# Kernel tuning notes

Measured on AMD Instinct MI355X. Metric: run time of the kernel, lower is better.

The kernel has to match this reference:

```python
import jax, jax.numpy as jnp
import numpy as np

N_NODES = 100000
N_EDGES = 1600000
D_IN = 256
D_OUT = 64
AVG_DEG = N_EDGES // N_NODES  # 16


def setup_inputs() -> dict:
    key = jax.random.key(0)
    k1, k2, k3 = jax.random.split(key, 3)
    X = jax.random.normal(k1, (N_NODES, D_IN), dtype=jnp.float32)
    weights = jax.random.normal(k2, (D_IN, D_OUT), dtype=jnp.float32) * (1.0 / np.sqrt(D_IN))
    # CSR with uniform degree for a valid structure (load balance is a kernel concern, not math)
    row_pointers = jnp.arange(N_NODES + 1, dtype=jnp.int64) * AVG_DEG
    column_index = jax.random.randint(k3, (N_EDGES,), 0, N_NODES, dtype=jnp.int64)
    # GNNAdvisor precomputes degrees as d^{-1/2} for symmetric GCN normalization
    deg = (row_pointers[1:] - row_pointers[:-1]).astype(jnp.float32)
    degrees = 1.0 / jnp.sqrt(jnp.maximum(deg, 1.0))
    return {"X": X, "weights": weights, "row_pointers": row_pointers,
            "column_index": column_index, "degrees": degrees}


def reference(X, weights, row_pointers, column_index, degrees):
    # Dense transform: [N, D_in] @ [D_in, D_out] -> [N, D_out]
    X_prime = jnp.matmul(X, weights)
    E = column_index.shape[0]
    # CSR row ids for each edge (destination node of the aggregation)
    row_ids = jnp.searchsorted(row_pointers, jnp.arange(E, dtype=row_pointers.dtype), side='right') - 1
    # out[i] = d_i^{-1/2} * sum_{j in N(i)} d_j^{-1/2} * X'[j]
    gathered = X_prime[column_index] * degrees[column_index][:, None]  # [E, D_out]
    agg = jax.ops.segment_sum(gathered, row_ids, num_segments=row_pointers.shape[0] - 1)
    return agg * degrees[:, None]
```

## Files before the change

### kernel.cpp

```cpp
#include <hip/hip_runtime.h>
#include <hip/hip_bf16.h>


constexpr int D_IN  = 256;
constexpr int D_OUT = 64;
constexpr int WT_LD = D_IN + 8;

typedef short  s8v  __attribute__((ext_vector_type(8)));
typedef __bf16 bf8v __attribute__((ext_vector_type(8)));
typedef float  f32x4 __attribute__((ext_vector_type(4)));
typedef unsigned short us8v __attribute__((ext_vector_type(8)));

union BF8 { bf8v b; s8v s; };

__global__ void prep_w_kernel(const float* __restrict__ W,
                              unsigned short* __restrict__ Wt_g)
{
    const int c = blockIdx.x;
    const int k = threadIdx.x;
    __bf16 b = (__bf16)W[(size_t)k * D_OUT + c];
    Wt_g[(size_t)c * D_IN + k] = *reinterpret_cast<unsigned short*>(&b);
}

__global__ __launch_bounds__(256) void gemm_bf16_kernel(
    const float* __restrict__ X, const unsigned short* __restrict__ Wt_g,
    const float* __restrict__ deg, unsigned short* __restrict__ Xp,
    int n, int ntiles)
{
    __shared__ unsigned short Wt[D_OUT][WT_LD];

    const int tid = threadIdx.x;

    {
        const int c = tid >> 2, seg = tid & 3;
        const us8v* src = reinterpret_cast<const us8v*>(Wt_g + (size_t)c * D_IN + seg * 64);
        us8v* dst = reinterpret_cast<us8v*>(&Wt[c][seg * 64]);
        #pragma unroll
        for (int i = 0; i < 8; ++i) dst[i] = src[i];
    }
    __syncthreads();

    const int wid  = tid >> 6;
    const int lane = tid & 63;
    const int lrow = lane & 15;
    const int kgrp = lane >> 4;

    const unsigned short* wt0 = &Wt[lrow][kgrp * 8];
    const int wstride = gridDim.x << 2;

    for (int tile = blockIdx.x * 4 + wid; tile < ntiles; tile += wstride) {
        const int grow = tile * 16 + lrow;
        const int xr   = grow < n ? grow : n - 1;
        const float* xrow = X + (size_t)xr * D_IN + kgrp * 8;

        f32x4 acc[4] = {};

        #pragma unroll
        for (int ks = 0; ks < 8; ++ks) {
            const float4 x0 = *reinterpret_cast<const float4*>(xrow + ks * 32);
            const float4 x1 = *reinterpret_cast<const float4*>(xrow + ks * 32 + 4);
            BF8 xf;
            xf.b[0] = (__bf16)x0.x; xf.b[1] = (__bf16)x0.y;
            xf.b[2] = (__bf16)x0.z; xf.b[3] = (__bf16)x0.w;
            xf.b[4] = (__bf16)x1.x; xf.b[5] = (__bf16)x1.y;
            xf.b[6] = (__bf16)x1.z; xf.b[7] = (__bf16)x1.w;

            #pragma unroll
            for (int f = 0; f < 4; ++f) {
                const s8v wf = *reinterpret_cast<const s8v*>(
                    wt0 + (size_t)f * 16 * WT_LD + ks * 32);
                acc[f] = __builtin_amdgcn_mfma_f32_16x16x32_bf16(wf, xf.s, acc[f], 0, 0, 0);
            }
        }

        if (grow < n) {
            const float d = deg[grow];
            #pragma unroll
            for (int f = 0; f < 4; ++f) {
                ushort4 v;
                __bf16 b0 = (__bf16)(acc[f][0] * d);
                __bf16 b1 = (__bf16)(acc[f][1] * d);
                __bf16 b2 = (__bf16)(acc[f][2] * d);
                __bf16 b3 = (__bf16)(acc[f][3] * d);
                v.x = *reinterpret_cast<unsigned short*>(&b0);
                v.y = *reinterpret_cast<unsigned short*>(&b1);
                v.z = *reinterpret_cast<unsigned short*>(&b2);
                v.w = *reinterpret_cast<unsigned short*>(&b3);
                *reinterpret_cast<ushort4*>(
                    &Xp[(size_t)grow * D_OUT + f * 16 + kgrp * 4]) = v;
            }
        }
    }
}

__global__ __launch_bounds__(256) void agg_kernel(
    const unsigned short* __restrict__ Xp, const int* __restrict__ rp,
    const int* __restrict__ ci, const float* __restrict__ deg,
    float* __restrict__ out, int n)
{
    const int node = blockIdx.x * 32 + (threadIdx.x >> 3);
    if (node >= n) return;
    const int c8 = (threadIdx.x & 7) * 8;

    const int e0 = rp[node];
    const int e1 = rp[node + 1];
    const int m  = e1 - e0;

    float acc[8] = {};

    if (m == 16 && (e0 & 3) == 0) {
        int4 i4[4];
        #pragma unroll
        for (int b = 0; b < 4; ++b)
            i4[b] = *reinterpret_cast<const int4*>(&ci[e0 + b * 4]);
        const int idx[16] = { i4[0].x, i4[0].y, i4[0].z, i4[0].w,
                              i4[1].x, i4[1].y, i4[1].z, i4[1].w,
                              i4[2].x, i4[2].y, i4[2].z, i4[2].w,
                              i4[3].x, i4[3].y, i4[3].z, i4[3].w };
        us8v v[16];
        #pragma unroll
        for (int j = 0; j < 16; ++j)
            v[j] = *reinterpret_cast<const us8v*>(&Xp[(size_t)idx[j] * D_OUT + c8]);
        #pragma unroll
        for (int j = 0; j < 16; ++j) {
            #pragma unroll
            for (int k = 0; k < 8; ++k)
                acc[k] += __uint_as_float((unsigned)v[j][k] << 16);
        }
    } else {
        for (int e = e0; e < e1; ++e) {
            const us8v v = *reinterpret_cast<const us8v*>(&Xp[(size_t)ci[e] * D_OUT + c8]);
            #pragma unroll
            for (int k = 0; k < 8; ++k)
                acc[k] += __uint_as_float((unsigned)v[k] << 16);
        }
    }

    const float d = deg[node];
    float* op = out + (size_t)node * D_OUT + c8;
    *reinterpret_cast<float4*>(op)     = make_float4(acc[0]*d, acc[1]*d, acc[2]*d, acc[3]*d);
    *reinterpret_cast<float4*>(op + 4) = make_float4(acc[4]*d, acc[5]*d, acc[6]*d, acc[7]*d);
}

extern "C" void kernel_launch(void* const* d_in, const int* in_sizes, int n_in,
                              void* d_out, int out_size, void* d_ws, size_t ws_size,
                              hipStream_t stream)
{
    const float* X   = (const float*)d_in[0];
    const float* W   = (const float*)d_in[1];
    const int*   rp  = (const int*)d_in[2];
    const int*   ci  = (const int*)d_in[3];
    const float* deg = (const float*)d_in[4];
    float* out = (float*)d_out;

    const int n = in_sizes[4];

    unsigned short* Xp   = (unsigned short*)d_ws;
    unsigned short* Wt_g = (unsigned short*)((char*)d_ws + (16u << 20));

    prep_w_kernel<<<D_OUT, D_IN, 0, stream>>>(W, Wt_g);

    const int ntiles = (n + 15) / 16;
    gemm_bf16_kernel<<<391, 256, 0, stream>>>(X, Wt_g, deg, Xp, n, ntiles);

    const int agg_blocks = (n + 31) / 32;
    agg_kernel<<<agg_blocks, 256, 0, stream>>>(Xp, rp, ci, deg, out, n);
}
```

Before: 60.36 us.

## Pre-swizzle weights into MFMA fragment order and load via global_load_lds

The weight prep kernel now writes bf16 weights in the exact per-lane MFMA fragment layout, so the GEMM kernel can copy them straight into LDS with global_load_lds and read conflict-free contiguous 16-byte fragments. The GEMM switches from a persistent grid-stride loop to one tile per wave with a launch sized to the tile count, and issues all 16 X float4 loads up front before converting and multiplying. This aims to raise memory-level parallelism on the X stream and cut LDS staging overhead, in exchange for more blocks each reloading the 32KB weight tile into LDS. The agg kernel also hoists the degree load earlier.

After: 59.00 us. 1.02x faster.

```diff
diff --git a/kernel.cpp b/kernel.cpp
--- a/kernel.cpp
+++ b/kernel.cpp
@@ -4,7 +4,6 @@
 
 constexpr int D_IN  = 256;
 constexpr int D_OUT = 64;
-constexpr int WT_LD = D_IN + 8;
 
 typedef short  s8v  __attribute__((ext_vector_type(8)));
 typedef __bf16 bf8v __attribute__((ext_vector_type(8)));
@@ -16,10 +15,20 @@
 __global__ void prep_w_kernel(const float* __restrict__ W,
                               unsigned short* __restrict__ Wt_g)
 {
-    const int c = blockIdx.x;
-    const int k = threadIdx.x;
-    __bf16 b = (__bf16)W[(size_t)k * D_OUT + c];
-    Wt_g[(size_t)c * D_IN + k] = *reinterpret_cast<unsigned short*>(&b);
+    const int t     = blockIdx.x * 256 + threadIdx.x;
+    const int lane  = t & 63;
+    const int chunk = t >> 6;
+    const int ks    = chunk >> 2;
+    const int f     = chunk & 3;
+    const int col   = f * 16 + (lane & 15);
+    const int k0    = (lane >> 4) * 8 + ks * 32;
+    us8v v;
+    #pragma unroll
+    for (int i = 0; i < 8; ++i) {
+        __bf16 b = (__bf16)W[(size_t)(k0 + i) * D_OUT + col];
+        v[i] = *reinterpret_cast<unsigned short*>(&b);
+    }
+    *reinterpret_cast<us8v*>(Wt_g + (size_t)t * 8) = v;
 }
 
 __global__ __launch_bounds__(256) void gemm_bf16_kernel(
@@ -27,68 +36,73 @@
     const float* __restrict__ deg, unsigned short* __restrict__ Xp,
     int n, int ntiles)
 {
-    __shared__ unsigned short Wt[D_OUT][WT_LD];
+    __shared__ unsigned short Wt[32 * 512];
 
-    const int tid = threadIdx.x;
+    const int tid  = threadIdx.x;
+    const int wid  = tid >> 6;
+    const int lane = tid & 63;
 
-    {
-        const int c = tid >> 2, seg = tid & 3;
-        const us8v* src = reinterpret_cast<const us8v*>(Wt_g + (size_t)c * D_IN + seg * 64);
-        us8v* dst = reinterpret_cast<us8v*>(&Wt[c][seg * 64]);
-        #pragma unroll
-        for (int i = 0; i < 8; ++i) dst[i] = src[i];
+    #pragma unroll
+    for (int c = 0; c < 8; ++c) {
+        const int chunk = wid * 8 + c;
+        const unsigned short* src = Wt_g + (size_t)chunk * 512 + lane * 8;
+        __builtin_amdgcn_global_load_lds(
+            (const __attribute__((address_space(1))) void*)src,
+            (__attribute__((address_space(3))) void*)&Wt[chunk * 512],
+            16, 0, 0);
     }
     __syncthreads();
 
-    const int wid  = tid >> 6;
-    const int lane = tid & 63;
+    const int tile = blockIdx.x * 4 + wid;
+    if (tile >= ntiles) return;
+
     const int lrow = lane & 15;
     const int kgrp = lane >> 4;
+    const int grow = tile * 16 + lrow;
+    const int xr   = grow < n ? grow : n - 1;
+    const float* xrow = X + (size_t)xr * D_IN + kgrp * 8;
 
-    const unsigned short* wt0 = &Wt[lrow][kgrp * 8];
-    const int wstride = gridDim.x << 2;
+    float4 xv[16];
+    #pragma unroll
+    for (int ks = 0; ks < 8; ++ks) {
+        xv[2 * ks]     = *reinterpret_cast<const float4*>(xrow + ks * 32);
+        xv[2 * ks + 1] = *reinterpret_cast<const float4*>(xrow + ks * 32 + 4);
+    }
 
-    for (int tile = blockIdx.x * 4 + wid; tile < ntiles; tile += wstride) {
-        const int grow = tile * 16 + lrow;
-        const int xr   = grow < n ? grow : n - 1;
-        const float* xrow = X + (size_t)xr * D_IN + kgrp * 8;
-
-        f32x4 acc[4] = {};
+    f32x4 acc[4] = {};
+    #pragma unroll
+    for (int ks = 0; ks < 8; ++ks) {
+        BF8 xf;
+        const float4 x0 = xv[2 * ks];
+        const float4 x1 = xv[2 * ks + 1];
+        xf.b[0] = (__bf16)x0.x; xf.b[1] = (__bf16)x0.y;
+        xf.b[2] = (__bf16)x0.z; xf.b[3] = (__bf16)x0.w;
+        xf.b[4] = (__bf16)x1.x; xf.b[5] = (__bf16)x1.y;
+        xf.b[6] = (__bf16)x1.z; xf.b[7] = (__bf16)x1.w;
 
         #pragma unroll
-        for (int ks = 0; ks < 8; ++ks) {
-            const float4 x0 = *reinterpret_cast<const float4*>(xrow + ks * 32);
-            const float4 x1 = *reinterpret_cast<const float4*>(xrow + ks * 32 + 4);
-            BF8 xf;
-            xf.b[0] = (__bf16)x0.x; xf.b[1] = (__bf16)x0.y;
-            xf.b[2] = (__bf16)x0.z; xf.b[3] = (__bf16)x0.w;
-            xf.b[4] = (__bf16)x1.x; xf.b[5] = (__bf16)x1.y;
-            xf.b[6] = (__bf16)x1.z; xf.b[7] = (__bf16)x1.w;
+        for (int f = 0; f < 4; ++f) {
+            const s8v wf = *reinterpret_cast<const s8v*>(
+                &Wt[(ks * 4 + f) * 512 + lane * 8]);
+            acc[f] = __builtin_amdgcn_mfma_f32_16x16x32_bf16(wf, xf.s, acc[f], 0, 0, 0);
+        }
+    }
 
-            #pragma unroll
-            for (int f = 0; f < 4; ++f) {
-                const s8v wf = *reinterpret_cast<const s8v*>(
-                    wt0 + (size_t)f * 16 * WT_LD + ks * 32);
-                acc[f] = __builtin_amdgcn_mfma_f32_16x16x32_bf16(wf, xf.s, acc[f], 0, 0, 0);
-            }
-        }
-
-        if (grow < n) {
-            const float d = deg[grow];
-            #pragma unroll
-            for (int f = 0; f < 4; ++f) {
-                ushort4 v;
-                __bf16 b0 = (__bf16)(acc[f][0] * d);
-                __bf16 b1 = (__bf16)(acc[f][1] * d);
-                __bf16 b2 = (__bf16)(acc[f][2] * d);
-                __bf16 b3 = (__bf16)(acc[f][3] * d);
-                v.x = *reinterpret_cast<unsigned short*>(&b0);
-                v.y = *reinterpret_cast<unsigned short*>(&b1);
-                v.z = *reinterpret_cast<unsigned short*>(&b2);
-                v.w = *reinterpret_cast<unsigned short*>(&b3);
-                *reinterpret_cast<ushort4*>(
-                    &Xp[(size_t)grow * D_OUT + f * 16 + kgrp * 4]) = v;
-            }
+    if (grow < n) {
+        const float d = deg[grow];
+        #pragma unroll
+        for (int f = 0; f < 4; ++f) {
+            ushort4 v;
+            __bf16 b0 = (__bf16)(acc[f][0] * d);
+            __bf16 b1 = (__bf16)(acc[f][1] * d);
+            __bf16 b2 = (__bf16)(acc[f][2] * d);
+            __bf16 b3 = (__bf16)(acc[f][3] * d);
+            v.x = *reinterpret_cast<unsigned short*>(&b0);
+            v.y = *reinterpret_cast<unsigned short*>(&b1);
+            v.z = *reinterpret_cast<unsigned short*>(&b2);
+            v.w = *reinterpret_cast<unsigned short*>(&b3);
+            *reinterpret_cast<ushort4*>(
+                &Xp[(size_t)grow * D_OUT + f * 16 + kgrp * 4]) = v;
         }
     }
 }
@@ -105,6 +119,7 @@
     const int e0 = rp[node];
     const int e1 = rp[node + 1];
     const int m  = e1 - e0;
+    const float d = deg[node];
 
     float acc[8] = {};
 
@@ -136,7 +151,6 @@
         }
     }
 
-    const float d = deg[node];
     float* op = out + (size_t)node * D_OUT + c8;
     *reinterpret_cast<float4*>(op)     = make_float4(acc[0]*d, acc[1]*d, acc[2]*d, acc[3]*d);
     *reinterpret_cast<float4*>(op + 4) = make_float4(acc[4]*d, acc[5]*d, acc[6]*d, acc[7]*d);
@@ -158,10 +172,11 @@
     unsigned short* Xp   = (unsigned short*)d_ws;
     unsigned short* Wt_g = (unsigned short*)((char*)d_ws + (16u << 20));
 
-    prep_w_kernel<<<D_OUT, D_IN, 0, stream>>>(W, Wt_g);
+    prep_w_kernel<<<8, 256, 0, stream>>>(W, Wt_g);
 
     const int ntiles = (n + 15) / 16;
-    gemm_bf16_kernel<<<391, 256, 0, stream>>>(X, Wt_g, deg, Xp, n, ntiles);
+    const int gemm_blocks = (ntiles + 3) / 4;
+    gemm_bf16_kernel<<<gemm_blocks, 256, 0, stream>>>(X, Wt_g, deg, Xp, n, ntiles);
 
     const int agg_blocks = (n + 31) / 32;
     agg_kernel<<<agg_blocks, 256, 0, stream>>>(Xp, rp, ci, deg, out, n);
```
